# Performance work log

Hardware: AMD Instinct MI355X
Metric: run time of the kernel (lower is better)

## Reference

```python
import jax, jax.numpy as jnp
import numpy as np

NT, NX = 64, 64
N_HALF = NT * NX // 2  # 2048 sites per checkerboard half

# mask[:, ::2] = False -> True at odd-x columns (the 'A' half)
_mask = np.ones((NT, NX), dtype=bool)
_mask[:, ::2] = False
IDX_A = jnp.asarray(np.where(_mask.reshape(-1))[0])   # [N_HALF]
IDX_B = jnp.asarray(np.where(~_mask.reshape(-1))[0])  # [N_HALF]


def setup_inputs() -> dict:
    key = jax.random.key(0)
    k0, k1, k2, k3, k4 = jax.random.split(key, 5)
    B = 4096
    scale = 1.0 / np.sqrt(N_HALF)
    return {
        "input_phi": jax.random.normal(k0, (B, NT, NX), dtype=jnp.float32),
        "W_s": jax.random.normal(k1, (N_HALF, N_HALF), dtype=jnp.float32) * scale,
        "b_s": jnp.zeros((N_HALF,), dtype=jnp.float32),
        "W_t": jax.random.normal(k2, (N_HALF, N_HALF), dtype=jnp.float32) * scale,
        "b_t": jnp.zeros((N_HALF,), dtype=jnp.float32),
    }


def _coupling(A, B, W_s, b_s, W_t, b_t):
    # Affine coupling: A' = A * exp(s(B)) + t(B); logDetJ = sum(s(B))
    s = jnp.tanh(B @ W_s.T + b_s)   # [batch, N_HALF]
    t = B @ W_t.T + b_t             # [batch, N_HALF]
    return A * jnp.exp(s) + t, jnp.sum(s, axis=-1)


def reference(input_phi, W_s, b_s, W_t, b_t):
    lead = input_phi.shape[:-2]
    phi = input_phi.reshape(*lead, NT * NX)
    A = phi[..., IDX_A]  # [batch, N_HALF]
    B = phi[..., IDX_B]
    A, logDetJc1 = _coupling(A, B, W_s, b_s, W_t, b_t)
    B, logDetJc2 = _coupling(B, A, W_s, b_s, W_t, b_t)
    out = jnp.zeros_like(phi).at[..., IDX_A].set(A).at[..., IDX_B].set(B)
    return out.reshape(*lead, NT, NX), logDetJc1 + logDetJc2
```

## Files before the change

kernel.cpp:

```cpp
#include <hip/hip_runtime.h>
#include <stdint.h>

#define BATCH 4096
#define NTX   4096
#define NH    2048
#define KDIM  2048

#define BM 128
#define BN 128
#define BK 32
#define TILE_E (BM * BK)

typedef __bf16 bf16x8 __attribute__((ext_vector_type(8)));
typedef float  f32x4  __attribute__((ext_vector_type(4)));

__device__ __forceinline__ unsigned short f2bf(float f) {
    union { float f; unsigned u; } v; v.f = f;
    unsigned u = v.u;
    unsigned r = u + 0x7fffu + ((u >> 16) & 1u);
    return (unsigned short)(r >> 16);
}

__device__ __forceinline__ float fast_tanh(float x) {
    float e = __expf(x + x);
    return 1.f - 2.f / (e + 1.f);
}

typedef __attribute__((address_space(1))) void gvoid;
typedef __attribute__((address_space(3))) void lvoid;

__device__ __forceinline__ void async16(const unsigned short* g, unsigned short* l) {
    __builtin_amdgcn_global_load_lds((gvoid*)(void*)g, (lvoid*)l, 16, 0, 0);
}

__device__ __forceinline__ int lds_off(int R, int c) {
    return R * BK + (((c) + (R >> 1)) & 3) * 8;
}

__global__ void prep(const float* __restrict__ phi,
                     const float* __restrict__ Wsf,
                     const float* __restrict__ Wtf,
                     unsigned short* __restrict__ Bbf,
                     unsigned short* __restrict__ Wsb,
                     unsigned short* __restrict__ Wtb,
                     float* __restrict__ out)
{
    const int tid    = blockIdx.x * blockDim.x + threadIdx.x;
    const int stride = gridDim.x * blockDim.x;

    const float4* p4 = (const float4*)phi;
    for (int i = tid; i < (BATCH * NH / 4); i += stride) {
        float4 u = p4[2 * i], v = p4[2 * i + 1];
        uint2 o;
        o.x = (unsigned)f2bf(u.x) | ((unsigned)f2bf(u.z) << 16);
        o.y = (unsigned)f2bf(v.x) | ((unsigned)f2bf(v.z) << 16);
        ((uint2*)Bbf)[i] = o;
    }

    const float4* ws4 = (const float4*)Wsf;
    const float4* wt4 = (const float4*)Wtf;
    for (int i = tid; i < (NH * KDIM / 8); i += stride) {
        float4 u = ws4[2 * i], v = ws4[2 * i + 1];
        uint4 o;
        o.x = (unsigned)f2bf(u.x) | ((unsigned)f2bf(u.y) << 16);
        o.y = (unsigned)f2bf(u.z) | ((unsigned)f2bf(u.w) << 16);
        o.z = (unsigned)f2bf(v.x) | ((unsigned)f2bf(v.y) << 16);
        o.w = (unsigned)f2bf(v.z) | ((unsigned)f2bf(v.w) << 16);
        ((uint4*)Wsb)[i] = o;
        u = wt4[2 * i]; v = wt4[2 * i + 1];
        o.x = (unsigned)f2bf(u.x) | ((unsigned)f2bf(u.y) << 16);
        o.y = (unsigned)f2bf(u.z) | ((unsigned)f2bf(u.w) << 16);
        o.z = (unsigned)f2bf(v.x) | ((unsigned)f2bf(v.y) << 16);
        o.w = (unsigned)f2bf(v.z) | ((unsigned)f2bf(v.w) << 16);
        ((uint4*)Wtb)[i] = o;
    }

    for (int i = tid; i < BATCH; i += stride) out[(size_t)BATCH * NTX + i] = 0.f;
}

__global__ __launch_bounds__(256, 2) void coupling_gemm(
    const unsigned short* __restrict__ X,
    const unsigned short* __restrict__ Wsb,
    const unsigned short* __restrict__ Wtb,
    const float* __restrict__ bs,
    const float* __restrict__ bt,
    const float* __restrict__ phi,
    float* __restrict__ out,
    unsigned short* __restrict__ Xout,
    int parity)
{
    __shared__ unsigned short lds[2][3][TILE_E];

    const int tid = threadIdx.x;
    const int m0 = blockIdx.x * BM;
    const int n0 = blockIdx.y * BN;

    f32x4 acc_s[4][4], acc_t[4][4];
    const f32x4 zf = {0.f, 0.f, 0.f, 0.f};
#pragma unroll
    for (int i = 0; i < 4; i++)
#pragma unroll
        for (int j = 0; j < 4; j++) { acc_s[i][j] = zf; acc_t[i][j] = zf; }

    const int rowA = tid >> 2;
    const int cgl  = (((tid & 3) - ((tid >> 3) & 3)) & 3) * 8;
    const unsigned short* Xg = X   + (size_t)(m0 + rowA) * KDIM + cgl;
    const unsigned short* Sg = Wsb + (size_t)(n0 + rowA) * KDIM + cgl;
    const unsigned short* Tg = Wtb + (size_t)(n0 + rowA) * KDIM + cgl;
    const size_t rstride = (size_t)64 * KDIM;
    const int lw = tid * 8;

    const int wave = tid >> 6;
    const int lane = tid & 63;
    const int wm = (wave >> 1) * 64;
    const int wn = (wave & 1) * 64;
    const int lrow = lane & 15;
    const int kc   = lane >> 4;

    {
        unsigned short* b = &lds[0][0][0];
        async16(Xg,           b + lw);
        async16(Xg + rstride, b + lw + 2048);
        b = &lds[0][1][0];
        async16(Sg,           b + lw);
        async16(Sg + rstride, b + lw + 2048);
        b = &lds[0][2][0];
        async16(Tg,           b + lw);
        async16(Tg + rstride, b + lw + 2048);
    }
    __syncthreads();

    const int NITER = KDIM / BK;
    for (int k = 0; k < NITER; k++) {
        const int cur = k & 1;
        const int nxt = cur ^ 1;
        {
            const int k0n = (k + 1 < NITER) ? (k + 1) * BK : 0;
            unsigned short* b = &lds[nxt][0][0];
            async16(Xg + k0n,           b + lw);
            async16(Xg + k0n + rstride, b + lw + 2048);
            b = &lds[nxt][1][0];
            async16(Sg + k0n,           b + lw);
            async16(Sg + k0n + rstride, b + lw + 2048);
            b = &lds[nxt][2][0];
            async16(Tg + k0n,           b + lw);
            async16(Tg + k0n + rstride, b + lw + 2048);
        }

        const unsigned short* Xs = &lds[cur][0][0];
        const unsigned short* Ss = &lds[cur][1][0];
        const unsigned short* Ts = &lds[cur][2][0];

        bf16x8 a[4], vs[4], vt[4];
#pragma unroll
        for (int i = 0; i < 4; i++) {
            a[i]  = *(const bf16x8*)(Xs + lds_off(wm + i * 16 + lrow, kc));
            vs[i] = *(const bf16x8*)(Ss + lds_off(wn + i * 16 + lrow, kc));
            vt[i] = *(const bf16x8*)(Ts + lds_off(wn + i * 16 + lrow, kc));
        }
#pragma unroll
        for (int mi = 0; mi < 4; mi++)
#pragma unroll
            for (int ni = 0; ni < 4; ni++) {
                acc_s[mi][ni] = __builtin_amdgcn_mfma_f32_16x16x32_bf16(
                    a[mi], vs[ni], acc_s[mi][ni], 0, 0, 0);
                acc_t[mi][ni] = __builtin_amdgcn_mfma_f32_16x16x32_bf16(
                    a[mi], vt[ni], acc_t[mi][ni], 0, 0, 0);
            }

        __syncthreads();
    }

    float* ldslot = out + (size_t)BATCH * NTX;
#pragma unroll
    for (int mi = 0; mi < 4; mi++) {
#pragma unroll
        for (int r = 0; r < 4; r++) {
            const int brow = m0 + wm + mi * 16 + (lane >> 4) * 4 + r;
            float ssum = 0.f;
#pragma unroll
            for (int ni = 0; ni < 4; ni++) {
                const int n = n0 + wn + ni * 16 + lrow;
                float s  = fast_tanh(acc_s[mi][ni][r] + bs[n]);
                float tv = acc_t[mi][ni][r] + bt[n];
                const size_t oidx = (size_t)brow * NTX + 2 * n + parity;
                float val = fmaf(phi[oidx], __expf(s), tv);
                out[oidx] = val;
                if (Xout) Xout[(size_t)brow * NH + n] = f2bf(val);
                ssum += s;
            }
            ssum += __shfl_xor(ssum, 1);
            ssum += __shfl_xor(ssum, 2);
            ssum += __shfl_xor(ssum, 4);
            ssum += __shfl_xor(ssum, 8);
            if (lrow == 0) atomicAdd(ldslot + brow, ssum);
        }
    }
}

extern "C" void kernel_launch(void* const* d_in, const int* in_sizes, int n_in,
                              void* d_out, int out_size, void* d_ws, size_t ws_size,
                              hipStream_t stream) {
    const float* phi = (const float*)d_in[0];
    const float* Wsf = (const float*)d_in[1];
    const float* bs  = (const float*)d_in[2];
    const float* Wtf = (const float*)d_in[3];
    const float* bt  = (const float*)d_in[4];
    float* out = (float*)d_out;

    char* ws = (char*)d_ws;
    unsigned short* Bbf  = (unsigned short*)(ws);
    unsigned short* Apbf = (unsigned short*)(ws + 16777216);
    unsigned short* Wsb  = (unsigned short*)(ws + 33554432);
    unsigned short* Wtb  = (unsigned short*)(ws + 41943040);

    prep<<<1024, 256, 0, stream>>>(phi, Wsf, Wtf, Bbf, Wsb, Wtb, out);

    coupling_gemm<<<dim3(32, 16), 256, 0, stream>>>(
        Bbf, Wsb, Wtb, bs, bt, phi, out, Apbf, 1);

    coupling_gemm<<<dim3(32, 16), 256, 0, stream>>>(
        Apbf, Wsb, Wtb, bs, bt, phi, out, nullptr, 0);
}
```

Measured before the change: 334.4 us.

## Enlarge GEMM tile to 256x128x64 with phased loads interleaved between MFMA stages

Grows the block tile to 256 rows by 128 columns with K-step 64, using 512 threads and a single combined LDS buffer per stage. A new 8-way XOR swizzle replaces the 4-way one. Each K-iteration is split into four MFMA phases, and the next tile's global-to-LDS loads are issued in chunks between them. Explicit vmcnt waits, barriers and setprio are used to overlap memory with compute. The aim is more data reuse per block and hidden load latency, at the cost of halving the grid (256 blocks), more barriers, and fragile hand-tuned waitcnt correctness.

Result: faster. 315.2 us (-5.7%).

```diff
diff --git a/kernel.cpp b/kernel.cpp
--- a/kernel.cpp
+++ b/kernel.cpp
@@ -6,10 +6,16 @@
 #define NH    2048
 #define KDIM  2048
 
-#define BM 128
+#define BM 256
 #define BN 128
-#define BK 32
-#define TILE_E (BM * BK)
+#define BK 64
+#define THREADS 512
+#define NITER (KDIM / BK)
+
+#define A_OFF 0
+#define S_OFF 16384
+#define T_OFF 24576
+#define BUF_E 32768
 
 typedef __bf16 bf16x8 __attribute__((ext_vector_type(8)));
 typedef float  f32x4  __attribute__((ext_vector_type(4)));
@@ -33,8 +39,8 @@
     __builtin_amdgcn_global_load_lds((gvoid*)(void*)g, (lvoid*)l, 16, 0, 0);
 }
 
-__device__ __forceinline__ int lds_off(int R, int c) {
-    return R * BK + (((c) + (R >> 1)) & 3) * 8;
+__device__ __forceinline__ int roff(int R, int c) {
+    return R * BK + (((c) + (R & 7)) & 7) * 8;
 }
 
 __global__ void prep(const float* __restrict__ phi,
@@ -78,7 +84,7 @@
     for (int i = tid; i < BATCH; i += stride) out[(size_t)BATCH * NTX + i] = 0.f;
 }
 
-__global__ __launch_bounds__(256, 2) void coupling_gemm(
+__global__ __launch_bounds__(THREADS, 2) void coupling_gemm(
     const unsigned short* __restrict__ X,
     const unsigned short* __restrict__ Wsb,
     const unsigned short* __restrict__ Wtb,
@@ -89,7 +95,7 @@
     unsigned short* __restrict__ Xout,
     int parity)
 {
-    __shared__ unsigned short lds[2][3][TILE_E];
+    __shared__ unsigned short lds[2][BUF_E];
 
     const int tid = threadIdx.x;
     const int m0 = blockIdx.x * BM;
@@ -102,12 +108,13 @@
 #pragma unroll
         for (int j = 0; j < 4; j++) { acc_s[i][j] = zf; acc_t[i][j] = zf; }
 
-    const int rowA = tid >> 2;
-    const int cgl  = (((tid & 3) - ((tid >> 3) & 3)) & 3) * 8;
-    const unsigned short* Xg = X   + (size_t)(m0 + rowA) * KDIM + cgl;
-    const unsigned short* Sg = Wsb + (size_t)(n0 + rowA) * KDIM + cgl;
-    const unsigned short* Tg = Wtb + (size_t)(n0 + rowA) * KDIM + cgl;
-    const size_t rstride = (size_t)64 * KDIM;
+    const int srow = tid >> 3;
+    const int cg   = ((tid & 7) - (srow & 7)) & 7;
+    const unsigned short* Ag = X   + (size_t)(m0 + srow) * KDIM + cg * 8;
+    const unsigned short* Sg = Wsb + (size_t)(n0 + srow) * KDIM + cg * 8;
+    const unsigned short* Tg = Wtb + (size_t)(n0 + srow) * KDIM + cg * 8;
+    const size_t r64  = (size_t)64  * KDIM;
+    const size_t r128 = (size_t)128 * KDIM;
     const int lw = tid * 8;
 
     const int wave = tid >> 6;
@@ -117,58 +124,104 @@
     const int lrow = lane & 15;
     const int kc   = lane >> 4;
 
+    int aO[4], sO[4], tO[4];
+#pragma unroll
+    for (int i = 0; i < 4; i++) {
+        aO[i] = A_OFF + roff(wm + i * 16 + lrow, kc);
+        sO[i] = S_OFF + roff(wn + i * 16 + lrow, kc);
+        tO[i] = T_OFF + roff(wn + i * 16 + lrow, kc);
+    }
+
     {
-        unsigned short* b = &lds[0][0][0];
-        async16(Xg,           b + lw);
-        async16(Xg + rstride, b + lw + 2048);
-        b = &lds[0][1][0];
-        async16(Sg,           b + lw);
-        async16(Sg + rstride, b + lw + 2048);
-        b = &lds[0][2][0];
-        async16(Tg,           b + lw);
-        async16(Tg + rstride, b + lw + 2048);
-    }
-    __syncthreads();
-
-    const int NITER = KDIM / BK;
-    for (int k = 0; k < NITER; k++) {
-        const int cur = k & 1;
-        const int nxt = cur ^ 1;
-        {
-            const int k0n = (k + 1 < NITER) ? (k + 1) * BK : 0;
-            unsigned short* b = &lds[nxt][0][0];
-            async16(Xg + k0n,           b + lw);
-            async16(Xg + k0n + rstride, b + lw + 2048);
-            b = &lds[nxt][1][0];
-            async16(Sg + k0n,           b + lw);
-            async16(Sg + k0n + rstride, b + lw + 2048);
-            b = &lds[nxt][2][0];
-            async16(Tg + k0n,           b + lw);
-            async16(Tg + k0n + rstride, b + lw + 2048);
+        unsigned short* b = &lds[0][0];
+        async16(Ag,              b + A_OFF + lw);
+        async16(Ag + r64,        b + A_OFF + 4096 + lw);
+        async16(Ag + r128,       b + A_OFF + 8192 + lw);
+        async16(Ag + r128 + r64, b + A_OFF + 12288 + lw);
+        async16(Sg,              b + S_OFF + lw);
+        async16(Sg + r64,        b + S_OFF + 4096 + lw);
+        async16(Tg,              b + T_OFF + lw);
+        async16(Tg + r64,        b + T_OFF + 4096 + lw);
+    }
+    asm volatile("s_waitcnt vmcnt(2)" ::: "memory");
+    __builtin_amdgcn_s_barrier();
+
+    for (int t = 0; t < NITER; ++t) {
+        unsigned short* bc = &lds[t & 1][0];
+        unsigned short* bx = &lds[(t & 1) ^ 1][0];
+        const int k0n = (((t + 1) < NITER) ? (t + 1) : 0) * BK;
+
+        bf16x8 a0[4], a1[4], f[4];
+
+#pragma unroll
+        for (int i = 0; i < 4; i++) {
+            a0[i] = *(const bf16x8*)(bc + aO[i]);
+            f[i]  = *(const bf16x8*)(bc + sO[i]);
         }
-
-        const unsigned short* Xs = &lds[cur][0][0];
-        const unsigned short* Ss = &lds[cur][1][0];
-        const unsigned short* Ts = &lds[cur][2][0];
-
-        bf16x8 a[4], vs[4], vt[4];
+        async16(Ag + k0n,       bx + A_OFF + lw);
+        async16(Ag + k0n + r64, bx + A_OFF + 4096 + lw);
+        __builtin_amdgcn_s_barrier();
+        __builtin_amdgcn_s_setprio(1);
+#pragma unroll
+        for (int mi = 0; mi < 4; mi++)
+#pragma unroll
+            for (int ni = 0; ni < 4; ni++)
+                acc_s[mi][ni] = __builtin_amdgcn_mfma_f32_16x16x32_bf16(
+                    a0[mi], f[ni], acc_s[mi][ni], 0, 0, 0);
+        __builtin_amdgcn_s_setprio(0);
+        __builtin_amdgcn_s_barrier();
+
 #pragma unroll
         for (int i = 0; i < 4; i++) {
-            a[i]  = *(const bf16x8*)(Xs + lds_off(wm + i * 16 + lrow, kc));
-            vs[i] = *(const bf16x8*)(Ss + lds_off(wn + i * 16 + lrow, kc));
-            vt[i] = *(const bf16x8*)(Ts + lds_off(wn + i * 16 + lrow, kc));
+            a1[i] = *(const bf16x8*)(bc + (aO[i] ^ 32));
+            f[i]  = *(const bf16x8*)(bc + (sO[i] ^ 32));
         }
-#pragma unroll
-        for (int mi = 0; mi < 4; mi++)
-#pragma unroll
-            for (int ni = 0; ni < 4; ni++) {
+        async16(Ag + k0n + r128,       bx + A_OFF + 8192 + lw);
+        async16(Ag + k0n + r128 + r64, bx + A_OFF + 12288 + lw);
+        __builtin_amdgcn_s_barrier();
+        __builtin_amdgcn_s_setprio(1);
+#pragma unroll
+        for (int mi = 0; mi < 4; mi++)
+#pragma unroll
+            for (int ni = 0; ni < 4; ni++)
                 acc_s[mi][ni] = __builtin_amdgcn_mfma_f32_16x16x32_bf16(
-                    a[mi], vs[ni], acc_s[mi][ni], 0, 0, 0);
+                    a1[mi], f[ni], acc_s[mi][ni], 0, 0, 0);
+        __builtin_amdgcn_s_setprio(0);
+        asm volatile("s_waitcnt vmcnt(4)" ::: "memory");
+        __builtin_amdgcn_s_barrier();
+
+#pragma unroll
+        for (int i = 0; i < 4; i++)
+            f[i] = *(const bf16x8*)(bc + tO[i]);
+        async16(Sg + k0n,       bx + S_OFF + lw);
+        async16(Sg + k0n + r64, bx + S_OFF + 4096 + lw);
+        __builtin_amdgcn_s_barrier();
+        __builtin_amdgcn_s_setprio(1);
+#pragma unroll
+        for (int mi = 0; mi < 4; mi++)
+#pragma unroll
+            for (int ni = 0; ni < 4; ni++)
                 acc_t[mi][ni] = __builtin_amdgcn_mfma_f32_16x16x32_bf16(
-                    a[mi], vt[ni], acc_t[mi][ni], 0, 0, 0);
-            }
-
-        __syncthreads();
+                    a0[mi], f[ni], acc_t[mi][ni], 0, 0, 0);
+        __builtin_amdgcn_s_setprio(0);
+        __builtin_amdgcn_s_barrier();
+
+#pragma unroll
+        for (int i = 0; i < 4; i++)
+            f[i] = *(const bf16x8*)(bc + (tO[i] ^ 32));
+        async16(Tg + k0n,       bx + T_OFF + lw);
+        async16(Tg + k0n + r64, bx + T_OFF + 4096 + lw);
+        __builtin_amdgcn_s_barrier();
+        __builtin_amdgcn_s_setprio(1);
+#pragma unroll
+        for (int mi = 0; mi < 4; mi++)
+#pragma unroll
+            for (int ni = 0; ni < 4; ni++)
+                acc_t[mi][ni] = __builtin_amdgcn_mfma_f32_16x16x32_bf16(
+                    a1[mi], f[ni], acc_t[mi][ni], 0, 0, 0);
+        __builtin_amdgcn_s_setprio(0);
+        asm volatile("s_waitcnt vmcnt(2)" ::: "memory");
+        __builtin_amdgcn_s_barrier();
     }
 
     float* ldslot = out + (size_t)BATCH * NTX;
@@ -216,9 +269,9 @@
 
     prep<<<1024, 256, 0, stream>>>(phi, Wsf, Wtf, Bbf, Wsb, Wtb, out);
 
-    coupling_gemm<<<dim3(32, 16), 256, 0, stream>>>(
+    coupling_gemm<<<dim3(16, 16), THREADS, 0, stream>>>(
         Bbf, Wsb, Wtb, bs, bt, phi, out, Apbf, 1);
 
-    coupling_gemm<<<dim3(32, 16), 256, 0, stream>>>(
+    coupling_gemm<<<dim3(16, 16), THREADS, 0, stream>>>(
         Apbf, Wsb, Wtb, bs, bt, phi, out, nullptr, 0);
 }
```
